# Optimization experiments

Measured on AMD Instinct MI355X. Metric: run time of the kernel, lower is better.

Reference implementation:

```python
import jax, jax.numpy as jnp
import numpy as np

N = 100000   # nodes
E = 1600000  # directed edges (self-loops appended in reference)
LRELU_SLOPE = 0.2
BN_EPS = 1e-5


def gat_layer(h_in, W, a_src, a_dst, bias, src, dst, heads, out_ch):
    """PyG-style GATConv (add_self_loops already applied to src/dst)."""
    n = h_in.shape[0]
    h = (h_in @ W.T).reshape(n, heads, out_ch)                 # [N,H,C]
    al_src = jnp.einsum('nhc,hc->nh', h, a_src)                # [N,H]
    al_dst = jnp.einsum('nhc,hc->nh', h, a_dst)
    e = jax.nn.leaky_relu(al_src[src] + al_dst[dst], LRELU_SLOPE)  # [Etot,H]
    # segment softmax over incoming edges of each destination node
    m = jax.ops.segment_max(e, dst, num_segments=n)
    ee = jnp.exp(e - m[dst])
    s = jax.ops.segment_sum(ee, dst, num_segments=n)
    alpha = ee / (s[dst] + 1e-16)                              # [Etot,H]
    out = jax.ops.segment_sum(h[src] * alpha[:, :, None], dst, num_segments=n)
    return out.reshape(n, heads * out_ch) + bias


def batchnorm_eval(x, gamma, beta, mean, var):
    return (x - mean) * jax.lax.rsqrt(var + BN_EPS) * gamma + beta


def setup_inputs() -> dict:
    key = jax.random.key(0)
    ks = jax.random.split(key, 30)
    d = {}
    d['x'] = jax.random.normal(ks[0], (N, 5), dtype=jnp.float32)
    d['edge_index'] = jax.random.randint(ks[1], (2, E), 0, N, dtype=jnp.int32)
    d['W1'] = jax.random.normal(ks[2], (64, 5), dtype=jnp.float32) * 0.3
    d['a1_src'] = jax.random.normal(ks[3], (4, 16), dtype=jnp.float32) * 0.3
    d['a1_dst'] = jax.random.normal(ks[4], (4, 16), dtype=jnp.float32) * 0.3
    d['b1'] = jax.random.normal(ks[5], (64,), dtype=jnp.float32) * 0.1
    d['W2'] = jax.random.normal(ks[6], (64, 64), dtype=jnp.float32) * 0.15
    d['a2_src'] = jax.random.normal(ks[7], (4, 16), dtype=jnp.float32) * 0.3
    d['a2_dst'] = jax.random.normal(ks[8], (4, 16), dtype=jnp.float32) * 0.3
    d['b2'] = jax.random.normal(ks[9], (64,), dtype=jnp.float32) * 0.1
    d['W3'] = jax.random.normal(ks[10], (64, 64), dtype=jnp.float32) * 0.15
    d['a3_src'] = jax.random.normal(ks[11], (1, 64), dtype=jnp.float32) * 0.2
    d['a3_dst'] = jax.random.normal(ks[12], (1, 64), dtype=jnp.float32) * 0.2
    d['b3'] = jax.random.normal(ks[13], (64,), dtype=jnp.float32) * 0.1
    d['bn_gamma'] = jax.random.uniform(ks[14], (3, 64), dtype=jnp.float32, minval=0.5, maxval=1.5)
    d['bn_beta'] = jax.random.normal(ks[15], (3, 64), dtype=jnp.float32) * 0.1
    d['bn_mean'] = jax.random.normal(ks[16], (3, 64), dtype=jnp.float32) * 0.1
    d['bn_var'] = jax.random.uniform(ks[17], (3, 64), dtype=jnp.float32, minval=0.5, maxval=1.5)
    d['clf_w1'] = jax.random.normal(ks[18], (32, 64), dtype=jnp.float32) * 0.15
    d['clf_b1'] = jax.random.normal(ks[19], (32,), dtype=jnp.float32) * 0.1
    d['clf_w2'] = jax.random.normal(ks[20], (3, 32), dtype=jnp.float32) * 0.2
    d['clf_b2'] = jax.random.normal(ks[21], (3,), dtype=jnp.float32) * 0.1
    d['reg_w1'] = jax.random.normal(ks[22], (32, 64), dtype=jnp.float32) * 0.15
    d['reg_b1'] = jax.random.normal(ks[23], (32,), dtype=jnp.float32) * 0.1
    d['reg_w2'] = jax.random.normal(ks[24], (1, 32), dtype=jnp.float32) * 0.2
    d['reg_b2'] = jax.random.normal(ks[25], (1,), dtype=jnp.float32) * 0.1
    return d


def reference(x, edge_index, W1, a1_src, a1_dst, b1, W2, a2_src, a2_dst, b2,
              W3, a3_src, a3_dst, b3, bn_gamma, bn_beta, bn_mean, bn_var,
              clf_w1, clf_b1, clf_w2, clf_b2, reg_w1, reg_b1, reg_w2, reg_b2):
    n = x.shape[0]
    loop = jnp.arange(n, dtype=edge_index.dtype)
    src = jnp.concatenate([edge_index[0], loop])
    dst = jnp.concatenate([edge_index[1], loop])

    h = gat_layer(x, W1, a1_src, a1_dst, b1, src, dst, 4, 16)
    h = jax.nn.elu(batchnorm_eval(h, bn_gamma[0], bn_beta[0], bn_mean[0], bn_var[0]))
    h = gat_layer(h, W2, a2_src, a2_dst, b2, src, dst, 4, 16)
    h = jax.nn.elu(batchnorm_eval(h, bn_gamma[1], bn_beta[1], bn_mean[1], bn_var[1]))
    h = gat_layer(h, W3, a3_src, a3_dst, b3, src, dst, 1, 64)
    h = batchnorm_eval(h, bn_gamma[2], bn_beta[2], bn_mean[2], bn_var[2])

    pooled = h.mean(axis=0, keepdims=True)                     # [1,64]
    hc = jax.nn.relu(pooled @ clf_w1.T + clf_b1)
    class_logits = hc @ clf_w2.T + clf_b2                      # [1,3]
    hr = jax.nn.relu(pooled @ reg_w1.T + reg_b1)
    rul_pred = hr @ reg_w2.T + reg_b2                          # [1,1]
    return class_logits, rul_pred
```

## Files before the change

kernel.cpp:

```cpp
#include <hip/hip_runtime.h>
#include <hip/hip_fp16.h>

#define LRELU_SLOPE 0.2f
#define BNEPS 1e-5f
#define BK 128
#define TILE 2048
#define CAPB 18432

__device__ __forceinline__ float lrelu(float x) { return x > 0.f ? x : LRELU_SLOPE * x; }

__global__ void k_init(int* __restrict__ cursorB, float* __restrict__ pooled) {
  int t = threadIdx.x;
  if (t < BK) cursorB[t] = t * CAPB;
  if (t < 64) pooled[t] = 0.f;
}

__global__ __launch_bounds__(256) void k_fat(
    const int* __restrict__ src, const int* __restrict__ dst,
    int* __restrict__ cursorB, int* __restrict__ stg, int E, int nbBucket,
    const float* __restrict__ x, const float* __restrict__ W,
    const float* __restrict__ asrc, const float* __restrict__ adst,
    __half* __restrict__ hg, float* __restrict__ alsrc, float* __restrict__ aldst, int N) {
  int t = threadIdx.x;
  if (blockIdx.x < nbBucket) {
    __shared__ int cnt[BK];
    __shared__ int off[BK];
    __shared__ int base[BK];
    __shared__ int pk[TILE];
    __shared__ int ga[TILE];
    int tb = blockIdx.x * TILE;

    for (int i = t; i < BK; i += 256) cnt[i] = 0;
    __syncthreads();

    int myp[8], myb[8], myrank[8];
#pragma unroll
    for (int k = 0; k < 8; ++k) {
      int e = tb + k * 256 + t;
      myb[k] = -1;
      if (e < E) {
        int s = src[e], d = dst[e];
        myp[k] = ((d & 1023) << 17) | s;
        myb[k] = d >> 10;
        myrank[k] = atomicAdd(&cnt[myb[k]], 1);
      }
    }
    __syncthreads();
    if (t < BK) off[t] = cnt[t];
    __syncthreads();
    for (int o = 1; o < BK; o <<= 1) {
      int xx = 0;
      if (t < BK && t >= o) xx = off[t - o];
      __syncthreads();
      if (t < BK) off[t] += xx;
      __syncthreads();
    }
    if (t < BK) {
      int c = cnt[t];
      off[t] -= c;
      base[t] = (c > 0) ? atomicAdd(&cursorB[t], c) : 0;
    }
    __syncthreads();
#pragma unroll
    for (int k = 0; k < 8; ++k) {
      if (myb[k] >= 0) {
        int p = off[myb[k]] + myrank[k];
        int a = base[myb[k]] + myrank[k];
        int lim = (myb[k] + 1) * CAPB;
        if (a >= lim) a = BK * CAPB + p;
        pk[p] = myp[k];
        ga[p] = a;
      }
    }
    __syncthreads();
    int nvalid = min(TILE, E - tb);
#pragma unroll
    for (int k = 0; k < 8; ++k) {
      int p = k * 256 + t;
      if (p < nvalid) stg[ga[p]] = pk[p];
    }
  } else {
    __shared__ float Ws[320];
    for (int i = t; i < 320; i += 256) Ws[i] = W[i];
    __syncthreads();
    int n = (blockIdx.x - nbBucket) * 4 + (t >> 6);
    int c = t & 63;
    if (n >= N) return;
    float acc = 0.f;
#pragma unroll
    for (int k = 0; k < 5; ++k) acc += x[n * 5 + k] * Ws[c * 5 + k];
    hg[(size_t)n * 64 + c] = __float2half_rn(acc);
    float ps = acc * asrc[c];
    float pd = acc * adst[c];
#pragma unroll
    for (int off = 1; off < 16; off <<= 1) {
      ps += __shfl_xor(ps, off, 64);
      pd += __shfl_xor(pd, off, 64);
    }
    if ((c & 15) == 0) {
      alsrc[n * 4 + (c >> 4)] = ps;
      aldst[n * 4 + (c >> 4)] = pd;
    }
  }
}

__global__ __launch_bounds__(1024) void k_fine(
    const int* __restrict__ stg, const int* __restrict__ cursorB,
    int* __restrict__ rowbeg, int* __restrict__ rowend, int* __restrict__ csr, int N) {
  __shared__ int cnt[1024];
  int b = blockIdx.x, t = threadIdx.x;
  int n0 = b << 10;
  int beg = b * CAPB;
  int end = min(cursorB[b], beg + CAPB);
  cnt[t] = 0;
  __syncthreads();
  for (int j = beg + t; j < end; j += 1024)
    atomicAdd(&cnt[stg[j] >> 17], 1);
  __syncthreads();
  int deg = cnt[t];
  for (int off = 1; off < 1024; off <<= 1) {
    int x = (t >= off) ? cnt[t - off] : 0;
    __syncthreads();
    cnt[t] += x;
    __syncthreads();
  }
  int rb = beg + cnt[t] - deg;
  int n = n0 + t;
  if (n < N) { rowbeg[n] = rb; rowend[n] = rb + deg; }
  __syncthreads();
  cnt[t] = rb;
  __syncthreads();
  for (int j = beg + t; j < end; j += 1024) {
    int e = stg[j];
    int pos = atomicAdd(&cnt[e >> 17], 1);
    csr[pos] = e & 0x1FFFF;
  }
}

template <int H>
__global__ __launch_bounds__(256) void k_gemm64(
    const __half* __restrict__ xin, const float* __restrict__ W,
    const float* __restrict__ asrc, const float* __restrict__ adst,
    __half* __restrict__ hg, float* __restrict__ alsrc, float* __restrict__ aldst, int N) {
  __shared__ float Xs[64 * 132];
  __shared__ float Ws[64 * 65];
  int t = threadIdx.x;
  int nb0 = blockIdx.x * 128;

  for (int idx = t; idx < 4096; idx += 256) {
    int c = idx >> 6, k = idx & 63;
    Ws[k * 65 + c] = W[idx];
  }
  {
    int n = t & 127, kh = t >> 7;
    int gn = nb0 + n;
#pragma unroll
    for (int j = 0; j < 4; ++j) {
      int col = kh * 32 + j * 8;
      float f[8];
      if (gn < N) {
        int4 raw = *(const int4*)&xin[(size_t)gn * 64 + col];
        const __half2* hp = (const __half2*)&raw;
#pragma unroll
        for (int i = 0; i < 4; ++i) {
          float2 f2 = __half22float2(hp[i]);
          f[i * 2] = f2.x; f[i * 2 + 1] = f2.y;
        }
      } else {
#pragma unroll
        for (int i = 0; i < 8; ++i) f[i] = 0.f;
      }
#pragma unroll
      for (int i = 0; i < 8; ++i) Xs[(col + i) * 132 + n] = f[i];
    }
  }
  __syncthreads();

  int cg = t & 7, ng = t >> 3;
  int c0 = cg * 8;
  float acc[4][8];
#pragma unroll
  for (int i = 0; i < 4; ++i)
#pragma unroll
    for (int j = 0; j < 8; ++j) acc[i][j] = 0.f;

  for (int k = 0; k < 64; ++k) {
    float4 xv = *(const float4*)&Xs[k * 132 + ng * 4];
    float w[8];
#pragma unroll
    for (int j = 0; j < 8; ++j) w[j] = Ws[k * 65 + c0 + j];
#pragma unroll
    for (int j = 0; j < 8; ++j) {
      acc[0][j] += xv.x * w[j];
      acc[1][j] += xv.y * w[j];
      acc[2][j] += xv.z * w[j];
      acc[3][j] += xv.w * w[j];
    }
  }

  float av[8], dv[8];
#pragma unroll
  for (int j = 0; j < 8; ++j) { av[j] = asrc[c0 + j]; dv[j] = adst[c0 + j]; }

#pragma unroll
  for (int i = 0; i < 4; ++i) {
    int n = nb0 + ng * 4 + i;
    float ps = 0.f, pd = 0.f;
#pragma unroll
    for (int j = 0; j < 8; ++j) { ps += acc[i][j] * av[j]; pd += acc[i][j] * dv[j]; }
    ps += __shfl_xor(ps, 1, 64);
    pd += __shfl_xor(pd, 1, 64);
    if (H == 1) {
      ps += __shfl_xor(ps, 2, 64); pd += __shfl_xor(pd, 2, 64);
      ps += __shfl_xor(ps, 4, 64); pd += __shfl_xor(pd, 4, 64);
    }
    if (n < N) {
      __half2 hv[4];
      hv[0] = __floats2half2_rn(acc[i][0], acc[i][1]);
      hv[1] = __floats2half2_rn(acc[i][2], acc[i][3]);
      hv[2] = __floats2half2_rn(acc[i][4], acc[i][5]);
      hv[3] = __floats2half2_rn(acc[i][6], acc[i][7]);
      *(float4*)&hg[(size_t)n * 64 + c0] = *(float4*)hv;
      if (H == 4) {
        if ((cg & 1) == 0) { alsrc[n * 4 + (cg >> 1)] = ps; aldst[n * 4 + (cg >> 1)] = pd; }
      } else {
        if (cg == 0) { alsrc[n] = ps; aldst[n] = pd; }
      }
    }
  }
}

template <int HEADS, bool DOELU>
__global__ __launch_bounds__(256) void k_agg(
    const __half* __restrict__ hg, const float* __restrict__ alsrc, const float* __restrict__ aldst,
    const int* __restrict__ rowbeg, const int* __restrict__ rowend, const int* __restrict__ csr,
    const float* __restrict__ bias, const float* __restrict__ gamma, const float* __restrict__ beta,
    const float* __restrict__ mean, const float* __restrict__ var,
    __half* __restrict__ out, int N) {
  int node = blockIdx.x * 4 + (threadIdx.x >> 6);
  if (node >= N) return;
  int lane = threadIdx.x & 63;
  int e16  = lane & 15;
  int gh   = (HEADS == 4) ? (lane >> 4) : 0;
  int c2   = lane & 31;
  int half = lane >> 5;
  int hc   = (HEADS == 4) ? (c2 >> 3) : 0;
  int psrc = hc * 16;

  float ad = aldst[node * HEADS + gh];
  float pself = __expf(lrelu(alsrc[node * HEADS + gh] + ad));
  float ssum = 0.f;

  float2 acc;
  {
    float pc = __shfl(pself, psrc, 64);
    float2 hf = __half22float2(*(const __half2*)&hg[(size_t)node * 64 + 2 * c2]);
    acc.x = (half == 0) ? pc * hf.x : 0.f;
    acc.y = (half == 0) ? pc * hf.y : 0.f;
  }

  int beg = rowbeg[node], end = rowend[node];
  for (int jb = beg; jb < end; jb += 16) {
    int j = jb + e16;
    int s = 0;
    float p = 0.f;
    if (j < end) {
      s = csr[j];
      p = __expf(lrelu(alsrc[s * HEADS + gh] + ad));
    }
    ssum += p;
#pragma unroll
    for (int e = 0; e < 16; e += 2) {
      int eslot = e + half;
      float pj = __shfl(p, psrc + eslot, 64);
      int   sj = __shfl(s, eslot, 64);
      float2 hf = __half22float2(*(const __half2*)&hg[(size_t)sj * 64 + 2 * c2]);
      acc.x += pj * hf.x;
      acc.y += pj * hf.y;
    }
  }
  ssum += __shfl_xor(ssum, 1, 64);
  ssum += __shfl_xor(ssum, 2, 64);
  ssum += __shfl_xor(ssum, 4, 64);
  ssum += __shfl_xor(ssum, 8, 64);
  float ssum_c = __shfl(ssum, psrc, 64) + __shfl(pself, psrc, 64);

  acc.x += __shfl_xor(acc.x, 32, 64);
  acc.y += __shfl_xor(acc.y, 32, 64);

  if (half == 0) {
    int c0 = 2 * c2;
    float2 bi = *(const float2*)&bias[c0];
    float2 mn = *(const float2*)&mean[c0];
    float2 vr = *(const float2*)&var[c0];
    float2 gm = *(const float2*)&gamma[c0];
    float2 bt = *(const float2*)&beta[c0];
    float inv = 1.f / (ssum_c + 1e-16f);
    float vx = acc.x * inv + bi.x;
    float vy = acc.y * inv + bi.y;
    vx = (vx - mn.x) * rsqrtf(vr.x + BNEPS) * gm.x + bt.x;
    vy = (vy - mn.y) * rsqrtf(vr.y + BNEPS) * gm.y + bt.y;
    if (DOELU) {
      vx = vx > 0.f ? vx : __expf(vx) - 1.f;
      vy = vy > 0.f ? vy : __expf(vy) - 1.f;
    }
    *(__half2*)&out[(size_t)node * 64 + c0] = __floats2half2_rn(vx, vy);
  }
}

__global__ void k_pool(const __half* __restrict__ h, float* __restrict__ pooled, int N) {
  __shared__ float red[4][64];
  int c = threadIdx.x & 63, r = threadIdx.x >> 6;
  float local = 0.f;
  for (int n = blockIdx.x * 4 + r; n < N; n += gridDim.x * 4)
    local += __half2float(h[(size_t)n * 64 + c]);
  red[r][c] = local;
  __syncthreads();
  if (r == 0) {
    float s = red[0][c] + red[1][c] + red[2][c] + red[3][c];
    atomicAdd(&pooled[c], s);
  }
}

__global__ void k_head(const float* __restrict__ pooled,
                       const float* __restrict__ cw1, const float* __restrict__ cb1,
                       const float* __restrict__ cw2, const float* __restrict__ cb2,
                       const float* __restrict__ rw1, const float* __restrict__ rb1,
                       const float* __restrict__ rw2, const float* __restrict__ rb2,
                       float* __restrict__ outp, float invN) {
  __shared__ float ps[64], hc[32], hr[32];
  int t = threadIdx.x;
  ps[t] = pooled[t] * invN;
  __syncthreads();
  if (t < 32) {
    float sc = cb1[t], sr = rb1[t];
    for (int c = 0; c < 64; ++c) {
      sc += ps[c] * cw1[t * 64 + c];
      sr += ps[c] * rw1[t * 64 + c];
    }
    hc[t] = sc > 0.f ? sc : 0.f;
    hr[t] = sr > 0.f ? sr : 0.f;
  }
  __syncthreads();
  if (t < 3) {
    float v = cb2[t];
    for (int j = 0; j < 32; ++j) v += hc[j] * cw2[t * 32 + j];
    outp[t] = v;
  } else if (t == 3) {
    float v = rb2[0];
    for (int j = 0; j < 32; ++j) v += hr[j] * rw2[j];
    outp[3] = v;
  }
}

static inline size_t align256(size_t x) { return (x + 255) & ~(size_t)255; }

extern "C" void kernel_launch(void* const* d_in, const int* in_sizes, int n_in,
                              void* d_out, int out_size, void* d_ws, size_t ws_size,
                              hipStream_t stream) {
  const float* x   = (const float*)d_in[0];
  const int*   ei  = (const int*)d_in[1];
  const float* W1  = (const float*)d_in[2];
  const float* a1s = (const float*)d_in[3];
  const float* a1d = (const float*)d_in[4];
  const float* b1  = (const float*)d_in[5];
  const float* W2  = (const float*)d_in[6];
  const float* a2s = (const float*)d_in[7];
  const float* a2d = (const float*)d_in[8];
  const float* b2  = (const float*)d_in[9];
  const float* W3  = (const float*)d_in[10];
  const float* a3s = (const float*)d_in[11];
  const float* a3d = (const float*)d_in[12];
  const float* b3  = (const float*)d_in[13];
  const float* bng = (const float*)d_in[14];
  const float* bnb = (const float*)d_in[15];
  const float* bnm = (const float*)d_in[16];
  const float* bnv = (const float*)d_in[17];
  const float* cw1 = (const float*)d_in[18];
  const float* cb1 = (const float*)d_in[19];
  const float* cw2 = (const float*)d_in[20];
  const float* cb2 = (const float*)d_in[21];
  const float* rw1 = (const float*)d_in[22];
  const float* rb1 = (const float*)d_in[23];
  const float* rw2 = (const float*)d_in[24];
  const float* rb2 = (const float*)d_in[25];

  const int N = in_sizes[0] / 5;
  const int E = in_sizes[1] / 2;
  const int* srcp = ei;
  const int* dstp = ei + E;
  const int NB = (N + 1023) >> 10;

  char* p = (char*)d_ws;
  int* rowbeg   = (int*)p;  p += align256((size_t)N * 4);
  int* rowend   = (int*)p;  p += align256((size_t)N * 4);
  int* csr      = (int*)p;  p += align256((size_t)BK * CAPB * 4);
  int* cursorB  = (int*)p;  p += align256(BK * 4);
  __half* hH    = (__half*)p; p += align256((size_t)N * 64 * 2);
  __half* hB    = (__half*)p; p += align256((size_t)N * 64 * 2);
  float* alsrc  = (float*)p;  p += align256((size_t)N * 4 * 4);
  float* aldst  = (float*)p;  p += align256((size_t)N * 4 * 4);
  float* pooled = (float*)p;  p += align256(64 * 4);
  int* stg      = (int*)p;    p += align256(((size_t)BK * CAPB + TILE) * 4);
  float* outp   = (float*)d_out;

  const int gNode4 = (N + 3) / 4;
  const int gNode128 = (N + 127) / 128;
  const int nbBucket = (E + TILE - 1) / TILE;

  k_init<<<1, 128, 0, stream>>>(cursorB, pooled);
  k_fat<<<nbBucket + gNode4, 256, 0, stream>>>(srcp, dstp, cursorB, stg, E, nbBucket,
      x, W1, a1s, a1d, hH, alsrc, aldst, N);
  k_fine<<<NB, 1024, 0, stream>>>(stg, cursorB, rowbeg, rowend, csr, N);

  k_agg<4, true><<<gNode4, 256, 0, stream>>>(hH, alsrc, aldst, rowbeg, rowend, csr,
      b1, bng + 0, bnb + 0, bnm + 0, bnv + 0, hB, N);

  k_gemm64<4><<<gNode128, 256, 0, stream>>>(hB, W2, a2s, a2d, hH, alsrc, aldst, N);
  k_agg<4, true><<<gNode4, 256, 0, stream>>>(hH, alsrc, aldst, rowbeg, rowend, csr,
      b2, bng + 64, bnb + 64, bnm + 64, bnv + 64, hB, N);

  k_gemm64<1><<<gNode128, 256, 0, stream>>>(hB, W3, a3s, a3d, hH, alsrc, aldst, N);
  k_agg<1, false><<<gNode4, 256, 0, stream>>>(hH, alsrc, aldst, rowbeg, rowend, csr,
      b3, bng + 128, bnb + 128, bnm + 128, bnv + 128, hB, N);

  k_pool<<<1024, 256, 0, stream>>>(hB, pooled, N);
  k_head<<<1, 64, 0, stream>>>(pooled, cw1, cb1, cw2, cb2, rw1, rb1, rw2, rb2,
                               outp, 1.0f / (float)N);
}
```

Baseline: 414.1 us.

## Move layer-1 GEMM into fine CSR kernel and replace init kernel with memset

Bucketing now runs alone, and the layer-1 node projection is folded into the fine-sort kernel as extra 1024-thread blocks, each handling 16 nodes. The cursor array now holds per-bucket offsets starting at zero, so a single hipMemsetAsync can clear the cursors and the pooled accumulator in place of the init kernel. This reshuffles which work runs concurrently and removes one launch, but the bucket pass no longer overlaps with the GEMM and the memset may carry its own overhead.

```diff
diff --git a/kernel.cpp b/kernel.cpp
--- a/kernel.cpp
+++ b/kernel.cpp
@@ -9,81 +9,110 @@
 
 __device__ __forceinline__ float lrelu(float x) { return x > 0.f ? x : LRELU_SLOPE * x; }
 
-__global__ void k_init(int* __restrict__ cursorB, float* __restrict__ pooled) {
+__global__ __launch_bounds__(256) void k_bucket(
+    const int* __restrict__ src, const int* __restrict__ dst,
+    int* __restrict__ cursorOff, int* __restrict__ stg, int E) {
+  __shared__ int cnt[BK];
+  __shared__ int off[BK];
+  __shared__ int base[BK];
+  __shared__ int pk[TILE];
+  __shared__ int ga[TILE];
   int t = threadIdx.x;
-  if (t < BK) cursorB[t] = t * CAPB;
-  if (t < 64) pooled[t] = 0.f;
-}
-
-__global__ __launch_bounds__(256) void k_fat(
-    const int* __restrict__ src, const int* __restrict__ dst,
-    int* __restrict__ cursorB, int* __restrict__ stg, int E, int nbBucket,
+  int tb = blockIdx.x * TILE;
+
+  for (int i = t; i < BK; i += 256) cnt[i] = 0;
+  __syncthreads();
+
+  int myp[8], myb[8], myrank[8];
+#pragma unroll
+  for (int k = 0; k < 8; ++k) {
+    int e = tb + k * 256 + t;
+    myb[k] = -1;
+    if (e < E) {
+      int s = src[e], d = dst[e];
+      myp[k] = ((d & 1023) << 17) | s;
+      myb[k] = d >> 10;
+      myrank[k] = atomicAdd(&cnt[myb[k]], 1);
+    }
+  }
+  __syncthreads();
+  if (t < BK) off[t] = cnt[t];
+  __syncthreads();
+  for (int o = 1; o < BK; o <<= 1) {
+    int xx = 0;
+    if (t < BK && t >= o) xx = off[t - o];
+    __syncthreads();
+    if (t < BK) off[t] += xx;
+    __syncthreads();
+  }
+  if (t < BK) {
+    int c = cnt[t];
+    off[t] -= c;
+    base[t] = t * CAPB + ((c > 0) ? atomicAdd(&cursorOff[t], c) : 0);
+  }
+  __syncthreads();
+#pragma unroll
+  for (int k = 0; k < 8; ++k) {
+    if (myb[k] >= 0) {
+      int p = off[myb[k]] + myrank[k];
+      int a = base[myb[k]] + myrank[k];
+      int lim = (myb[k] + 1) * CAPB;
+      if (a >= lim) a = BK * CAPB + p;
+      pk[p] = myp[k];
+      ga[p] = a;
+    }
+  }
+  __syncthreads();
+  int nvalid = min(TILE, E - tb);
+#pragma unroll
+  for (int k = 0; k < 8; ++k) {
+    int p = k * 256 + t;
+    if (p < nvalid) stg[ga[p]] = pk[p];
+  }
+}
+
+__global__ __launch_bounds__(1024) void k_finegemm(
+    const int* __restrict__ stg, const int* __restrict__ cursorOff,
+    int* __restrict__ rowbeg, int* __restrict__ rowend, int* __restrict__ csr,
+    int N, int NB,
     const float* __restrict__ x, const float* __restrict__ W,
     const float* __restrict__ asrc, const float* __restrict__ adst,
-    __half* __restrict__ hg, float* __restrict__ alsrc, float* __restrict__ aldst, int N) {
+    __half* __restrict__ hg, float* __restrict__ alsrc, float* __restrict__ aldst) {
   int t = threadIdx.x;
-  if (blockIdx.x < nbBucket) {
-    __shared__ int cnt[BK];
-    __shared__ int off[BK];
-    __shared__ int base[BK];
-    __shared__ int pk[TILE];
-    __shared__ int ga[TILE];
-    int tb = blockIdx.x * TILE;
-
-    for (int i = t; i < BK; i += 256) cnt[i] = 0;
-    __syncthreads();
-
-    int myp[8], myb[8], myrank[8];
-#pragma unroll
-    for (int k = 0; k < 8; ++k) {
-      int e = tb + k * 256 + t;
-      myb[k] = -1;
-      if (e < E) {
-        int s = src[e], d = dst[e];
-        myp[k] = ((d & 1023) << 17) | s;
-        myb[k] = d >> 10;
-        myrank[k] = atomicAdd(&cnt[myb[k]], 1);
-      }
-    }
-    __syncthreads();
-    if (t < BK) off[t] = cnt[t];
-    __syncthreads();
-    for (int o = 1; o < BK; o <<= 1) {
-      int xx = 0;
-      if (t < BK && t >= o) xx = off[t - o];
+  if (blockIdx.x < NB) {
+    __shared__ int cnt[1024];
+    int b = blockIdx.x;
+    int n0 = b << 10;
+    int beg = b * CAPB;
+    int end = beg + min(cursorOff[b], CAPB);
+    cnt[t] = 0;
+    __syncthreads();
+    for (int j = beg + t; j < end; j += 1024)
+      atomicAdd(&cnt[stg[j] >> 17], 1);
+    __syncthreads();
+    int deg = cnt[t];
+    for (int off = 1; off < 1024; off <<= 1) {
+      int xx = (t >= off) ? cnt[t - off] : 0;
       __syncthreads();
-      if (t < BK) off[t] += xx;
+      cnt[t] += xx;
       __syncthreads();
     }
-    if (t < BK) {
-      int c = cnt[t];
-      off[t] -= c;
-      base[t] = (c > 0) ? atomicAdd(&cursorB[t], c) : 0;
-    }
-    __syncthreads();
-#pragma unroll
-    for (int k = 0; k < 8; ++k) {
-      if (myb[k] >= 0) {
-        int p = off[myb[k]] + myrank[k];
-        int a = base[myb[k]] + myrank[k];
-        int lim = (myb[k] + 1) * CAPB;
-        if (a >= lim) a = BK * CAPB + p;
-        pk[p] = myp[k];
-        ga[p] = a;
-      }
-    }
-    __syncthreads();
-    int nvalid = min(TILE, E - tb);
-#pragma unroll
-    for (int k = 0; k < 8; ++k) {
-      int p = k * 256 + t;
-      if (p < nvalid) stg[ga[p]] = pk[p];
+    int rb = beg + cnt[t] - deg;
+    int n = n0 + t;
+    if (n < N) { rowbeg[n] = rb; rowend[n] = rb + deg; }
+    __syncthreads();
+    cnt[t] = rb;
+    __syncthreads();
+    for (int j = beg + t; j < end; j += 1024) {
+      int e = stg[j];
+      int pos = atomicAdd(&cnt[e >> 17], 1);
+      csr[pos] = e & 0x1FFFF;
     }
   } else {
     __shared__ float Ws[320];
-    for (int i = t; i < 320; i += 256) Ws[i] = W[i];
-    __syncthreads();
-    int n = (blockIdx.x - nbBucket) * 4 + (t >> 6);
+    for (int i = t; i < 320; i += 1024) Ws[i] = W[i];
+    __syncthreads();
+    int n = (blockIdx.x - NB) * 16 + (t >> 6);
     int c = t & 63;
     if (n >= N) return;
     float acc = 0.f;
@@ -101,39 +130,6 @@
       alsrc[n * 4 + (c >> 4)] = ps;
       aldst[n * 4 + (c >> 4)] = pd;
     }
-  }
-}
-
-__global__ __launch_bounds__(1024) void k_fine(
-    const int* __restrict__ stg, const int* __restrict__ cursorB,
-    int* __restrict__ rowbeg, int* __restrict__ rowend, int* __restrict__ csr, int N) {
-  __shared__ int cnt[1024];
-  int b = blockIdx.x, t = threadIdx.x;
-  int n0 = b << 10;
-  int beg = b * CAPB;
-  int end = min(cursorB[b], beg + CAPB);
-  cnt[t] = 0;
-  __syncthreads();
-  for (int j = beg + t; j < end; j += 1024)
-    atomicAdd(&cnt[stg[j] >> 17], 1);
-  __syncthreads();
-  int deg = cnt[t];
-  for (int off = 1; off < 1024; off <<= 1) {
-    int x = (t >= off) ? cnt[t - off] : 0;
-    __syncthreads();
-    cnt[t] += x;
-    __syncthreads();
-  }
-  int rb = beg + cnt[t] - deg;
-  int n = n0 + t;
-  if (n < N) { rowbeg[n] = rb; rowend[n] = rb + deg; }
-  __syncthreads();
-  cnt[t] = rb;
-  __syncthreads();
-  for (int j = beg + t; j < end; j += 1024) {
-    int e = stg[j];
-    int pos = atomicAdd(&cnt[e >> 17], 1);
-    csr[pos] = e & 0x1FFFF;
   }
 }
 
@@ -392,26 +388,28 @@
   const int NB = (N + 1023) >> 10;
 
   char* p = (char*)d_ws;
-  int* rowbeg   = (int*)p;  p += align256((size_t)N * 4);
-  int* rowend   = (int*)p;  p += align256((size_t)N * 4);
-  int* csr      = (int*)p;  p += align256((size_t)BK * CAPB * 4);
-  int* cursorB  = (int*)p;  p += align256(BK * 4);
+  int* rowbeg    = (int*)p;  p += align256((size_t)N * 4);
+  int* rowend    = (int*)p;  p += align256((size_t)N * 4);
+  int* csr       = (int*)p;  p += align256((size_t)BK * CAPB * 4);
+  int* cursorOff = (int*)p;
+  float* pooled  = (float*)(p + BK * 4);
+  p += align256(BK * 4 + 64 * 4);
   __half* hH    = (__half*)p; p += align256((size_t)N * 64 * 2);
   __half* hB    = (__half*)p; p += align256((size_t)N * 64 * 2);
   float* alsrc  = (float*)p;  p += align256((size_t)N * 4 * 4);
   float* aldst  = (float*)p;  p += align256((size_t)N * 4 * 4);
-  float* pooled = (float*)p;  p += align256(64 * 4);
   int* stg      = (int*)p;    p += align256(((size_t)BK * CAPB + TILE) * 4);
   float* outp   = (float*)d_out;
 
   const int gNode4 = (N + 3) / 4;
   const int gNode128 = (N + 127) / 128;
   const int nbBucket = (E + TILE - 1) / TILE;
-
-  k_init<<<1, 128, 0, stream>>>(cursorB, pooled);
-  k_fat<<<nbBucket + gNode4, 256, 0, stream>>>(srcp, dstp, cursorB, stg, E, nbBucket,
-      x, W1, a1s, a1d, hH, alsrc, aldst, N);
-  k_fine<<<NB, 1024, 0, stream>>>(stg, cursorB, rowbeg, rowend, csr, N);
+  const int gGemm1 = (N + 15) / 16;
+
+  hipMemsetAsync(cursorOff, 0, BK * 4 + 64 * 4, stream);
+  k_bucket<<<nbBucket, 256, 0, stream>>>(srcp, dstp, cursorOff, stg, E);
+  k_finegemm<<<NB + gGemm1, 1024, 0, stream>>>(stg, cursorOff, rowbeg, rowend, csr,
+      N, NB, x, W1, a1s, a1d, hH, alsrc, aldst);
 
   k_agg<4, true><<<gNode4, 256, 0, stream>>>(hH, alsrc, aldst, rowbeg, rowend, csr,
       b1, bng + 0, bnb + 0, bnm + 0, bnv + 0, hB, N);
```

Measured after the change: 401.8 us. 1.03x faster.
